# Performance work log

Hardware: AMD Instinct MI355X
Metric: run time of the kernel (lower is better)

The kernel has to match this reference:

```python
import jax, jax.numpy as jnp
import numpy as np

B, S, H, HF, V, L, NB, K = 8, 512, 1024, 512, 32000, 4, 8, 2
EPS = 1e-5


def _ln(x, g, b):
    m = jnp.mean(x, -1, keepdims=True)
    v = jnp.mean((x - m) ** 2, -1, keepdims=True)
    return (x - m) * jax.lax.rsqrt(v + EPS) * g + b


def setup_inputs() -> dict:
    key = jax.random.key(0)
    ks = jax.random.split(key, 12)
    n = lambda i, shape, s=0.02: jax.random.normal(ks[i], shape, jnp.float32) * s
    return {
        "input_ids": jax.random.randint(ks[0], (B, S), 0, V),
        "emb": n(1, (V, H)),
        "pos": n(2, (1, 512, H)),
        "torsion_field": jnp.zeros((1, H), jnp.float32),
        "lm_w": n(3, (H, V)),
        "lm_b": jnp.zeros((V,), jnp.float32),
        "sel_w": n(4, (L, H, NB)),
        "sel_b": jnp.zeros((L, NB), jnp.float32),
        "g1": jnp.ones((L, NB, H), jnp.float32),
        "b1": jnp.zeros((L, NB, H), jnp.float32),
        "attn_w": n(5, (L, NB, H, H)),
        "attn_b": jnp.zeros((L, NB, H), jnp.float32),
        "g2": jnp.ones((L, NB, H), jnp.float32),
        "b2": jnp.zeros((L, NB, H), jnp.float32),
        "ff1_w": n(6, (L, NB, H, HF)),
        "ff1_b": jnp.zeros((L, NB, HF), jnp.float32),
        "ff2_w": n(7, (L, NB, HF, H)),
        "ff2_b": jnp.zeros((L, NB, H), jnp.float32),
        "tg": n(8, (L, NB, H), 0.01),
    }


def _forward(input_ids, emb, pos, torsion_field, lm_w, lm_b, sel_w, sel_b,
             g1, b1, attn_w, attn_b, g2, b2, ff1_w, ff1_b, ff2_w, ff2_b, tg):
    # embedding + positional encoding
    h = emb[input_ids] + pos[:, :input_ids.shape[1], :]        # [B,S,H]
    tf = torsion_field[0]                                      # [H] (zeros buffer)
    PRIORITY = 0.5  # fresh block: success_rate*0.6 + excitement*0.4 = 0.5
    for l in range(L):
        # router: sigmoid(Linear(mean-pooled x)), mixed with block priority; topk on batch row 0
        scores = jax.nn.sigmoid(jnp.mean(h, 1) @ sel_w[l] + sel_b[l])   # [B,NB]
        adj0 = scores[0] * 0.7 + PRIORITY * 0.3                         # [NB]
        _, top_idx = jax.lax.top_k(adj0, K)                             # [K]
        params = jax.tree_util.tree_map(
            lambda p: p[l][top_idx],
            (g1, b1, attn_w, attn_b, g2, b2, ff1_w, ff1_b, ff2_w, ff2_b, tg))

        def blk(carry, p):
            pg1, pb1, pwa, pba, pg2, pb2, pw1, pbf1, pw2, pbf2, ptg = p
            x = carry
            ha = _ln(x, pg1, pb1) @ pwa + pba                           # [B,S,H]
            ha = ha * (1.0 + jax.nn.sigmoid(ptg) * tf)[None, None, :]
            hm = x + 0.5 * ha
            h2 = _ln(hm, pg2, pb2)
            h2 = jax.nn.gelu(h2 @ pw1 + pbf1, approximate=False) @ pw2 + pbf2
            return hm + 0.5 * h2, None

        h, _ = jax.lax.scan(blk, h, params)
        h = 1.5 * h  # h*0.5 + h after each layer
    return h @ lm_w + lm_b                                     # [B,S,V]


def reference(input_ids, emb, pos, torsion_field, lm_w, lm_b, sel_w, sel_b,
              g1, b1, attn_w, attn_b, g2, b2, ff1_w, ff1_b, ff2_w, ff2_b, tg):
    return _forward(input_ids, emb, pos, torsion_field, lm_w, lm_b, sel_w, sel_b,
                    g1, b1, attn_w, attn_b, g2, b2, ff1_w, ff1_b, ff2_w, ff2_b, tg)
```

## Files before the change

kernel.cpp:

```cpp
#include <hip/hip_runtime.h>


typedef unsigned short u16;
typedef short bf16x8 __attribute__((ext_vector_type(8)));
typedef float f32x4 __attribute__((ext_vector_type(4)));

struct __align__(8) u16x4_t { u16 x, y, z, w; };

#define MTOT 4096
#define HDIM 1024
#define HFF  512
#define VOC  32000
#define NLAYER 4
#define NBLK 8

#define VMW(n) asm volatile("s_waitcnt vmcnt(" #n ")" ::: "memory")
#define BARR() do { asm volatile("" ::: "memory"); __builtin_amdgcn_s_barrier(); asm volatile("" ::: "memory"); } while (0)

__device__ __forceinline__ u16 f2bf(float f) {
  unsigned u = __float_as_uint(f);
  unsigned r = u + 0x7FFFu + ((u >> 16) & 1u);
  return (u16)(r >> 16);
}

__device__ __forceinline__ float b2f(u16 v) {
  return __uint_as_float(((unsigned)v) << 16);
}

__device__ __forceinline__ float sigmoidf_(float z) {
  return 1.0f / (1.0f + expf(-z));
}

__device__ __forceinline__ void gload16(const void* g, void* l) {
  __builtin_amdgcn_global_load_lds(
      (const __attribute__((address_space(1))) void*)g,
      (__attribute__((address_space(3))) void*)l, 16, 0, 0);
}

__global__ void embed_lm_kernel(const int* __restrict__ ids,
                                const float* __restrict__ emb,
                                const float* __restrict__ pos,
                                u16* __restrict__ x,
                                const float* __restrict__ lm_w,
                                u16* __restrict__ lmT) {
  __shared__ float tile[32][33];
  int b = blockIdx.x, tid = threadIdx.x;
  if (b < MTOT) {
    int s = b & 511;
    int id = ids[b];
    float4 e = ((const float4*)(emb + (size_t)id * HDIM))[tid];
    float4 p = ((const float4*)(pos + (size_t)s * HDIM))[tid];
    u16x4_t r;
    r.x = f2bf(e.x + p.x); r.y = f2bf(e.y + p.y);
    r.z = f2bf(e.z + p.z); r.w = f2bf(e.w + p.w);
    ((u16x4_t*)(x + (size_t)b * HDIM))[tid] = r;
    return;
  }
  int c = b - MTOT;
  int n0 = (c % 1000) * 32, k0 = (c / 1000) * 32;
  int tx = tid & 31, ty = tid >> 5;
#pragma unroll
  for (int j = 0; j < 4; ++j) {
    int kr = k0 + ty + j * 8;
    tile[ty + j * 8][tx] = lm_w[(size_t)kr * VOC + n0 + tx];
  }
  __syncthreads();
#pragma unroll
  for (int j = 0; j < 4; ++j) {
    int nr = n0 + ty + j * 8;
    lmT[(size_t)nr * HDIM + k0 + tx] = f2bf(tile[tx][ty + j * 8]);
  }
}

__global__ void colsum_kernel(const u16* __restrict__ x, float* __restrict__ partial) {
  int j = blockIdx.x;
  int t = threadIdx.x;
  float4 s; s.x = 0.f; s.y = 0.f; s.z = 0.f; s.w = 0.f;
  for (int r = 0; r < 8; ++r) {
    u16x4_t a = ((const u16x4_t*)(x + (size_t)(j * 8 + r) * HDIM))[t];
    s.x += b2f(a.x); s.y += b2f(a.y); s.z += b2f(a.z); s.w += b2f(a.w);
  }
  ((float4*)(partial + (size_t)j * HDIM))[t] = s;
}

__global__ void router_finalize(const float* __restrict__ partial,
                                const float* __restrict__ selw,
                                const float* __restrict__ selb,
                                const float* __restrict__ tg_l,
                                const float* __restrict__ tf,
                                int* __restrict__ idx_out,
                                float* __restrict__ scale_out) {
  int t = threadIdx.x;
  float s = 0.f;
  for (int j = 0; j < 64; ++j) s += partial[(size_t)j * HDIM + t];
  float mean = s * (1.0f / 512.0f);
  __shared__ float sm[HDIM];
  __shared__ float sc[NBLK];
  __shared__ int sidx[2];
  sm[t] = mean;
  __syncthreads();
  int wave = t >> 6, lane = t & 63;
  if (wave < NBLK) {
    float p = 0.f;
    for (int h = lane; h < HDIM; h += 64) p += sm[h] * selw[h * NBLK + wave];
    for (int o = 32; o; o >>= 1) p += __shfl_down(p, o);
    if (lane == 0) sc[wave] = p;
  }
  __syncthreads();
  if (t == 0) {
    float adj[NBLK];
    for (int i = 0; i < NBLK; ++i) {
      float z = sc[i] + selb[i];
      adj[i] = sigmoidf_(z) * 0.7f + 0.15f;
    }
    int i0 = 0;
    for (int i = 1; i < NBLK; ++i) if (adj[i] > adj[i0]) i0 = i;
    int i1 = -1;
    for (int i = 0; i < NBLK; ++i) {
      if (i == i0) continue;
      if (i1 < 0 || adj[i] > adj[i1]) i1 = i;
    }
    idx_out[0] = i0; idx_out[1] = i1;
    sidx[0] = i0; sidx[1] = i1;
  }
  __syncthreads();
  for (int k = 0; k < 2; ++k) {
    int id = sidx[k];
    float z = tg_l[(size_t)id * HDIM + t];
    scale_out[k * HDIM + t] = 1.0f + sigmoidf_(z) * tf[t];
  }
}

__global__ void prep_kernel(const float* __restrict__ aw,
                            const float* __restrict__ f1w,
                            const float* __restrict__ f2w,
                            const int* __restrict__ idx, int slot,
                            u16* __restrict__ wA, u16* __restrict__ w1,
                            u16* __restrict__ w2,
                            const u16* __restrict__ x,
                            const float* __restrict__ g_base,
                            const float* __restrict__ b_base,
                            u16* __restrict__ abf) {
  __shared__ float sh[32 * 33];
  int b = blockIdx.x, tid = threadIdx.x;
  int id = idx[slot];
  if (b < 2048) {
    float (*tile)[33] = (float(*)[33])sh;
    const float* src; u16* dst; int K, N, n0, k0;
    if (b < 1024) {
      K = 1024; N = 1024; src = aw + (size_t)id * 1024 * 1024;
      n0 = (b & 31) * 32; k0 = (b >> 5) * 32; dst = wA;
    } else if (b < 1536) {
      int c = b - 1024; K = 1024; N = 512; src = f1w + (size_t)id * 1024 * 512;
      n0 = (c & 15) * 32; k0 = (c >> 4) * 32; dst = w1;
    } else {
      int c = b - 1536; K = 512; N = 1024; src = f2w + (size_t)id * 512 * 1024;
      n0 = (c & 31) * 32; k0 = (c >> 5) * 32; dst = w2;
    }
    int tx = tid & 31, ty = tid >> 5;
#pragma unroll
    for (int j = 0; j < 4; ++j) {
      int kr = k0 + ty + j * 8;
      tile[ty + j * 8][tx] = src[(size_t)kr * N + n0 + tx];
    }
    __syncthreads();
#pragma unroll
    for (int j = 0; j < 4; ++j) {
      int nr = n0 + ty + j * 8;
      dst[(size_t)nr * K + k0 + tx] = f2bf(tile[tx][ty + j * 8]);
    }
    return;
  }
  int row = b - 2048, t = tid;
  const float* g = g_base + (size_t)id * HDIM;
  const float* bb = b_base + (size_t)id * HDIM;
  u16x4_t xv = ((const u16x4_t*)(x + (size_t)row * HDIM))[t];
  float v0 = b2f(xv.x), v1 = b2f(xv.y), v2 = b2f(xv.z), v3 = b2f(xv.w);
  float s = v0 + v1 + v2 + v3;
  float q = v0 * v0 + v1 * v1 + v2 * v2 + v3 * v3;
  for (int o = 32; o; o >>= 1) { s += __shfl_down(s, o); q += __shfl_down(q, o); }
  float* ss = sh; float* sq = sh + 8;
  int wave = t >> 6, lane = t & 63;
  if (lane == 0) { ss[wave] = s; sq[wave] = q; }
  __syncthreads();
  if (t == 0) {
    float S = ss[0] + ss[1] + ss[2] + ss[3];
    float Q = sq[0] + sq[1] + sq[2] + sq[3];
    ss[0] = S * (1.0f / 1024.0f);
    sq[0] = Q * (1.0f / 1024.0f);
  }
  __syncthreads();
  float mean = ss[0];
  float var = sq[0] - mean * mean;
  float rs = rsqrtf(var + 1e-5f);
  float4 gv = ((const float4*)g)[t];
  float4 bv = ((const float4*)bb)[t];
  u16x4_t o4;
  o4.x = f2bf((v0 - mean) * rs * gv.x + bv.x);
  o4.y = f2bf((v1 - mean) * rs * gv.y + bv.y);
  o4.z = f2bf((v2 - mean) * rs * gv.z + bv.z);
  o4.w = f2bf((v3 - mean) * rs * gv.w + bv.w);
  ((u16x4_t*)(abf + (size_t)row * HDIM))[t] = o4;
}

__global__ void ln_kernel(const u16* __restrict__ x,
                          const float* __restrict__ g_base,
                          const float* __restrict__ b_base,
                          const int* __restrict__ idx_ptr, int slot,
                          u16* __restrict__ out) {
  int row = blockIdx.x, t = threadIdx.x;
  size_t off = (size_t)idx_ptr[slot] * HDIM;
  const float* g = g_base + off;
  const float* b = b_base + off;
  u16x4_t xv = ((const u16x4_t*)(x + (size_t)row * HDIM))[t];
  float v0 = b2f(xv.x), v1 = b2f(xv.y), v2 = b2f(xv.z), v3 = b2f(xv.w);
  float s = v0 + v1 + v2 + v3;
  float q = v0 * v0 + v1 * v1 + v2 * v2 + v3 * v3;
  for (int o = 32; o; o >>= 1) { s += __shfl_down(s, o); q += __shfl_down(q, o); }
  __shared__ float ss[4], sq[4];
  int wave = t >> 6, lane = t & 63;
  if (lane == 0) { ss[wave] = s; sq[wave] = q; }
  __syncthreads();
  if (t == 0) {
    float S = ss[0] + ss[1] + ss[2] + ss[3];
    float Q = sq[0] + sq[1] + sq[2] + sq[3];
    ss[0] = S * (1.0f / 1024.0f);
    sq[0] = Q * (1.0f / 1024.0f);
  }
  __syncthreads();
  float mean = ss[0];
  float var = sq[0] - mean * mean;
  float rs = rsqrtf(var + 1e-5f);
  float4 gv = ((const float4*)g)[t];
  float4 bv = ((const float4*)b)[t];
  u16x4_t o4;
  o4.x = f2bf((v0 - mean) * rs * gv.x + bv.x);
  o4.y = f2bf((v1 - mean) * rs * gv.y + bv.y);
  o4.z = f2bf((v2 - mean) * rs * gv.z + bv.z);
  o4.w = f2bf((v3 - mean) * rs * gv.w + bv.w);
  ((u16x4_t*)(out + (size_t)row * HDIM))[t] = o4;
}

template <int BM, int BN, int EPI>
__global__ __launch_bounds__(256) void gemm_layer(
    const u16* __restrict__ A, const u16* __restrict__ Bt, int N, int K,
    const float* __restrict__ bias_base, const int* __restrict__ idx_ptr,
    int slot, int bias_stride, const float* __restrict__ scale,
    u16* __restrict__ xres, u16* __restrict__ outb, float lscale) {
  constexpr int TM = BM / 2, TN = BN / 2;
  constexpr int FM = TM / 16, FN = TN / 16;
  constexpr int NLD = (BM + BN) / 16;
  __shared__ __align__(16) u16 lds[(BM + BN) * 128];

  const int tid = threadIdx.x, wave = tid >> 6, lane = tid & 63;
  const int m0 = blockIdx.y * BM, n0 = blockIdx.x * BN;
  const int wm = wave >> 1, wn = wave & 1;
  const int fr = lane & 15, g = lane >> 4;
  const float* bias =
      bias_base + (idx_ptr ? (size_t)idx_ptr[slot] * bias_stride : 0);

  const u16* gbase[NLD];
  unsigned ldsoff[NLD];
#pragma unroll
  for (int j = 0; j < NLD; ++j) {
    int lo = (tid + j * 256) * 16;
    int q = (lo >> 4) & 15;
    if (lo < BM * 256) {
      int row = lo >> 8;
      gbase[j] = A + (size_t)(m0 + row) * K + (q ^ (row & 7)) * 8;
    } else {
      int bo = lo - BM * 256;
      int row = bo >> 8;
      gbase[j] = Bt + (size_t)(n0 + row) * K + (q ^ (row & 7)) * 8;
    }
    ldsoff[j] = (unsigned)(lo >> 1);
  }

  unsigned offA[FM][4], offB[FN][4];
#pragma unroll
  for (int mi = 0; mi < FM; ++mi)
#pragma unroll
    for (int kk = 0; kk < 4; ++kk)
      offA[mi][kk] = (unsigned)((wm * TM + mi * 16 + fr) * 256 +
                                (((kk * 4 + g) ^ (fr & 7)) << 4));
#pragma unroll
  for (int ni = 0; ni < FN; ++ni)
#pragma unroll
    for (int kk = 0; kk < 4; ++kk)
      offB[ni][kk] = (unsigned)(BM * 256 + (wn * TN + ni * 16 + fr) * 256 +
                                (((kk * 4 + g) ^ (fr & 7)) << 4));

  f32x4 acc[FM][FN];
#pragma unroll
  for (int i = 0; i < FM; ++i)
#pragma unroll
    for (int j = 0; j < FN; ++j) acc[i][j] = (f32x4){0.f, 0.f, 0.f, 0.f};

  for (int kt = 0; kt < K; kt += 128) {
#pragma unroll
    for (int j = 0; j < NLD; ++j) gload16(gbase[j] + kt, lds + ldsoff[j]);
    __syncthreads();
#pragma unroll
    for (int kk = 0; kk < 4; ++kk) {
      bf16x8 af[FM], bf[FN];
#pragma unroll
      for (int mi = 0; mi < FM; ++mi)
        af[mi] = *(const bf16x8*)((const char*)lds + offA[mi][kk]);
#pragma unroll
      for (int ni = 0; ni < FN; ++ni)
        bf[ni] = *(const bf16x8*)((const char*)lds + offB[ni][kk]);
#pragma unroll
      for (int mi = 0; mi < FM; ++mi)
#pragma unroll
        for (int ni = 0; ni < FN; ++ni)
          acc[mi][ni] = __builtin_amdgcn_mfma_f32_16x16x32_bf16(
              af[mi], bf[ni], acc[mi][ni], 0, 0, 0);
    }
    __syncthreads();
  }

  const int rb = g * 4, cn = fr;
  float bvv[FN], svv[FN];
#pragma unroll
  for (int ni = 0; ni < FN; ++ni) {
    int n = n0 + wn * TN + ni * 16 + cn;
    bvv[ni] = bias[n];
    svv[ni] = (EPI == 0) ? scale[n] : 0.f;
  }
#pragma unroll
  for (int mi = 0; mi < FM; ++mi) {
#pragma unroll
    for (int r = 0; r < 4; ++r) {
      int m = m0 + wm * TM + mi * 16 + rb + r;
      size_t base = (size_t)m * N + n0 + wn * TN + cn;
#pragma unroll
      for (int ni = 0; ni < FN; ++ni) {
        float c = acc[mi][ni][r] + bvv[ni];
        size_t o = base + ni * 16;
        if (EPI == 0) {
          float xv = b2f(xres[o]);
          xres[o] = f2bf(xv + 0.5f * (c * svv[ni]));
        } else if (EPI == 1) {
          float ge = 0.5f * c * (1.0f + erff(c * 0.70710678118654752f));
          outb[o] = f2bf(ge);
        } else {
          float xv = b2f(xres[o]);
          xres[o] = f2bf((xv + 0.5f * c) * lscale);
        }
      }
    }
  }
}

__global__ __launch_bounds__(512, 2) void gemm_lm(
    const u16* __restrict__ A, const u16* __restrict__ Bt,
    const float* __restrict__ bias, float* __restrict__ out) {
  constexpr int K = HDIM;
  constexpr int N = VOC;
  constexpr int NT = K / 64;
  __shared__ __align__(16) u16 smbuf[2 * 32768];

  const int tid = threadIdx.x, wid = tid >> 6, lane = tid & 63;
  const int bid = blockIdx.x;
  const int vbid = (bid & 7) * 250 + (bid >> 3);
  const int n0 = (vbid >> 4) * 256;
  const int m0 = (vbid & 15) * 256;
  const int wm = wid >> 2, wn = wid & 3;
  const int fr = lane & 15, g = lane >> 4;

  const int r0 = tid >> 3, q = tid & 7;
  const int sg = (q ^ (r0 & 7)) * 8;
  const u16* usrc[4][2];
  unsigned uoff[4][2];
  usrc[0][0] = Bt + (size_t)(n0 + r0) * K + sg;        uoff[0][0] = 16384u + tid * 8;
  usrc[0][1] = Bt + (size_t)(n0 + 64 + r0) * K + sg;   uoff[0][1] = 20480u + tid * 8;
  usrc[1][0] = Bt + (size_t)(n0 + 128 + r0) * K + sg;  uoff[1][0] = 24576u + tid * 8;
  usrc[1][1] = Bt + (size_t)(n0 + 192 + r0) * K + sg;  uoff[1][1] = 28672u + tid * 8;
  usrc[2][0] = A + (size_t)(m0 + r0) * K + sg;         uoff[2][0] = 0u + tid * 8;
  usrc[2][1] = A + (size_t)(m0 + 128 + r0) * K + sg;   uoff[2][1] = 8192u + tid * 8;
  usrc[3][0] = A + (size_t)(m0 + 64 + r0) * K + sg;    uoff[3][0] = 4096u + tid * 8;
  usrc[3][1] = A + (size_t)(m0 + 192 + r0) * K + sg;   uoff[3][1] = 12288u + tid * 8;

  unsigned offA[8][2], offB[4][2];
#pragma unroll
  for (int mi = 0; mi < 8; ++mi)
#pragma unroll
    for (int kk = 0; kk < 2; ++kk)
      offA[mi][kk] = (unsigned)((wm * 128 + mi * 16 + fr) * 128 +
                                (((kk * 4 + g) ^ (fr & 7)) << 4));
#pragma unroll
  for (int ni = 0; ni < 4; ++ni)
#pragma unroll
    for (int kk = 0; kk < 2; ++kk)
      offB[ni][kk] = (unsigned)(32768 + (wn * 64 + ni * 16 + fr) * 128 +
                                (((kk * 4 + g) ^ (fr & 7)) << 4));

  f32x4 acc[8][4];
#pragma unroll
  for (int i = 0; i < 8; ++i)
#pragma unroll
    for (int j = 0; j < 4; ++j) acc[i][j] = (f32x4){0.f, 0.f, 0.f, 0.f};

#pragma unroll
  for (int u = 0; u < 4; ++u) {
    gload16(usrc[u][0], smbuf + uoff[u][0]);
    gload16(usrc[u][1], smbuf + uoff[u][1]);
  }

  for (int t = 0; t < NT; ++t) {
    const char* cb = (const char*)smbuf + (size_t)(t & 1) * 65536;
    u16* nb = smbuf + ((t + 1) & 1) * 32768;
    const int ko = (t + 1) * 64;
    const bool st = (t + 1 < NT);
    bf16x8 avl[4], avh[4], bv[4];
    VMW(2);
    BARR();
#pragma unroll
    for (int ni = 0; ni < 4; ++ni) bv[ni] = *(const bf16x8*)(cb + offB[ni][0]);
#pragma unroll
    for (int mi = 0; mi < 4; ++mi) avl[mi] = *(const bf16x8*)(cb + offA[mi][0]);
    if (st) {
      gload16(usrc[0][0] + ko, nb + uoff[0][0]);
      gload16(usrc[0][1] + ko, nb + uoff[0][1]);
    }
    __builtin_amdgcn_s_setprio(1);
#pragma unroll
    for (int mi = 0; mi < 4; ++mi)
#pragma unroll
      for (int ni = 0; ni < 4; ++ni)
        acc[mi][ni] = __builtin_amdgcn_mfma_f32_16x16x32_bf16(
            avl[mi], bv[ni], acc[mi][ni], 0, 0, 0);
    __builtin_amdgcn_s_setprio(0);
    if (t < NT - 1) { VMW(2); } else { VMW(0); }
    BARR();
#pragma unroll
    for (int mi = 0; mi < 4; ++mi)
      avh[mi] = *(const bf16x8*)(cb + offA[4 + mi][0]);
    if (st) {
      gload16(usrc[1][0] + ko, nb + uoff[1][0]);
      gload16(usrc[1][1] + ko, nb + uoff[1][1]);
    }
    __builtin_amdgcn_s_setprio(1);
#pragma unroll
    for (int mi = 0; mi < 4; ++mi)
#pragma unroll
      for (int ni = 0; ni < 4; ++ni)
        acc[4 + mi][ni] = __builtin_amdgcn_mfma_f32_16x16x32_bf16(
            avh[mi], bv[ni], acc[4 + mi][ni], 0, 0, 0);
    __builtin_amdgcn_s_setprio(0);
#pragma unroll
    for (int ni = 0; ni < 4; ++ni) bv[ni] = *(const bf16x8*)(cb + offB[ni][1]);
#pragma unroll
    for (int mi = 0; mi < 4; ++mi) avl[mi] = *(const bf16x8*)(cb + offA[mi][1]);
    if (st) {
      gload16(usrc[2][0] + ko, nb + uoff[2][0]);
      gload16(usrc[2][1] + ko, nb + uoff[2][1]);
    }
    __builtin_amdgcn_s_setprio(1);
#pragma unroll
    for (int mi = 0; mi < 4; ++mi)
#pragma unroll
      for (int ni = 0; ni < 4; ++ni)
        acc[mi][ni] = __builtin_amdgcn_mfma_f32_16x16x32_bf16(
            avl[mi], bv[ni], acc[mi][ni], 0, 0, 0);
    __builtin_amdgcn_s_setprio(0);
#pragma unroll
    for (int mi = 0; mi < 4; ++mi)
      avh[mi] = *(const bf16x8*)(cb + offA[4 + mi][1]);
    if (st) {
      gload16(usrc[3][0] + ko, nb + uoff[3][0]);
      gload16(usrc[3][1] + ko, nb + uoff[3][1]);
    }
    __builtin_amdgcn_s_setprio(1);
#pragma unroll
    for (int mi = 0; mi < 4; ++mi)
#pragma unroll
      for (int ni = 0; ni < 4; ++ni)
        acc[4 + mi][ni] = __builtin_amdgcn_mfma_f32_16x16x32_bf16(
            avh[mi], bv[ni], acc[4 + mi][ni], 0, 0, 0);
    __builtin_amdgcn_s_setprio(0);
  }

  const int rb = g * 4, cn = fr;
  float bvv[4];
#pragma unroll
  for (int ni = 0; ni < 4; ++ni) bvv[ni] = bias[n0 + wn * 64 + ni * 16 + cn];
#pragma unroll
  for (int mi = 0; mi < 8; ++mi) {
#pragma unroll
    for (int r = 0; r < 4; ++r) {
      int m = m0 + wm * 128 + mi * 16 + rb + r;
      float* orow = out + (size_t)m * N + n0 + wn * 64 + cn;
#pragma unroll
      for (int ni = 0; ni < 4; ++ni)
        __builtin_nontemporal_store(acc[mi][ni][r] + bvv[ni], orow + ni * 16);
    }
  }
}

extern "C" void kernel_launch(void* const* d_in, const int* in_sizes, int n_in,
                              void* d_out, int out_size, void* d_ws,
                              size_t ws_size, hipStream_t stream) {
  (void)in_sizes; (void)n_in; (void)out_size; (void)ws_size;
  const int*   ids    = (const int*)d_in[0];
  const float* emb    = (const float*)d_in[1];
  const float* pos    = (const float*)d_in[2];
  const float* tf     = (const float*)d_in[3];
  const float* lm_w   = (const float*)d_in[4];
  const float* lm_b   = (const float*)d_in[5];
  const float* sel_w  = (const float*)d_in[6];
  const float* sel_b  = (const float*)d_in[7];
  const float* g1     = (const float*)d_in[8];
  const float* b1     = (const float*)d_in[9];
  const float* attn_w = (const float*)d_in[10];
  const float* attn_b = (const float*)d_in[11];
  const float* g2     = (const float*)d_in[12];
  const float* b2     = (const float*)d_in[13];
  const float* ff1_w  = (const float*)d_in[14];
  const float* ff1_b  = (const float*)d_in[15];
  const float* ff2_w  = (const float*)d_in[16];
  const float* ff2_b  = (const float*)d_in[17];
  const float* tg     = (const float*)d_in[18];
  float* out = (float*)d_out;

  char* ws = (char*)d_ws;
  u16*   x       = (u16*)(ws + 0);
  u16*   abf     = (u16*)(ws + 16777216);
  u16*   tbuf    = (u16*)(ws + 25165824);
  u16*   wA      = (u16*)(ws + 29360128);
  u16*   w1      = (u16*)(ws + 31457280);
  u16*   w2      = (u16*)(ws + 32505856);
  u16*   lmT     = (u16*)(ws + 33554432);
  float* partial = (float*)(ws + 99090432);
  float* scalev  = (float*)(ws + 99352576);
  int*   idx     = (int*)(ws + 99360768);

  embed_lm_kernel<<<MTOT + VOC, 256, 0, stream>>>(ids, emb, pos, x, lm_w, lmT);

  for (int l = 0; l < NLAYER; ++l) {
    colsum_kernel<<<64, 256, 0, stream>>>(x, partial);
    router_finalize<<<1, 1024, 0, stream>>>(
        partial, sel_w + (size_t)l * HDIM * NBLK, sel_b + l * NBLK,
        tg + (size_t)l * NBLK * HDIM, tf, idx, scalev);
    const float* aw_l  = attn_w + (size_t)l * NBLK * HDIM * HDIM;
    const float* f1w_l = ff1_w + (size_t)l * NBLK * HDIM * HFF;
    const float* f2w_l = ff2_w + (size_t)l * NBLK * HFF * HDIM;
    for (int k = 0; k < 2; ++k) {
      prep_kernel<<<2048 + MTOT, 256, 0, stream>>>(
          aw_l, f1w_l, f2w_l, idx, k, wA, w1, w2, x,
          g1 + (size_t)l * NBLK * HDIM, b1 + (size_t)l * NBLK * HDIM, abf);
      gemm_layer<128, 64, 0><<<dim3(16, 32), 256, 0, stream>>>(
          abf, wA, HDIM, HDIM, attn_b + (size_t)l * NBLK * HDIM, idx, k, HDIM,
          scalev + k * HDIM, x, nullptr, 1.0f);
      ln_kernel<<<MTOT, 256, 0, stream>>>(x, g2 + (size_t)l * NBLK * HDIM,
                                          b2 + (size_t)l * NBLK * HDIM, idx, k,
                                          abf);
      gemm_layer<64, 64, 1><<<dim3(8, 64), 256, 0, stream>>>(
          abf, w1, HFF, HDIM, ff1_b + (size_t)l * NBLK * HFF, idx, k, HFF,
          nullptr, nullptr, tbuf, 1.0f);
      float lsc = (k == 1) ? 1.5f : 1.0f;
      gemm_layer<128, 64, 2><<<dim3(16, 32), 256, 0, stream>>>(
          tbuf, w2, HDIM, HFF, ff2_b + (size_t)l * NBLK * HDIM, idx, k, HDIM,
          nullptr, x, nullptr, lsc);
    }
  }

  gemm_lm<<<2000, 512, 0, stream>>>(x, lmT, lm_b, out);
}
```

Measured before the change: 931.7 us.

## Shrink LM-head GEMM tile to 128x128 with simpler double-buffered pipeline

```diff
diff --git a/kernel.cpp b/kernel.cpp
--- a/kernel.cpp
+++ b/kernel.cpp
@@ -352,133 +352,109 @@
   }
 }
 
-__global__ __launch_bounds__(512, 2) void gemm_lm(
+__global__ __launch_bounds__(256, 2) void gemm_lm(
     const u16* __restrict__ A, const u16* __restrict__ Bt,
     const float* __restrict__ bias, float* __restrict__ out) {
   constexpr int K = HDIM;
   constexpr int N = VOC;
   constexpr int NT = K / 64;
-  __shared__ __align__(16) u16 smbuf[2 * 32768];
-
-  const int tid = threadIdx.x, wid = tid >> 6, lane = tid & 63;
+  __shared__ __align__(16) u16 smbuf[2 * 16384];
+
+  const int tid = threadIdx.x, wave = tid >> 6, lane = tid & 63;
   const int bid = blockIdx.x;
-  const int vbid = (bid & 7) * 250 + (bid >> 3);
-  const int n0 = (vbid >> 4) * 256;
-  const int m0 = (vbid & 15) * 256;
-  const int wm = wid >> 2, wn = wid & 3;
+  const int vbid = (bid & 7) * 1000 + (bid >> 3);
+  const int n0 = (vbid >> 5) * 128;
+  const int m0 = (vbid & 31) * 128;
+  const int wm = wave >> 1, wn = wave & 1;
   const int fr = lane & 15, g = lane >> 4;
 
-  const int r0 = tid >> 3, q = tid & 7;
-  const int sg = (q ^ (r0 & 7)) * 8;
-  const u16* usrc[4][2];
-  unsigned uoff[4][2];
-  usrc[0][0] = Bt + (size_t)(n0 + r0) * K + sg;        uoff[0][0] = 16384u + tid * 8;
-  usrc[0][1] = Bt + (size_t)(n0 + 64 + r0) * K + sg;   uoff[0][1] = 20480u + tid * 8;
-  usrc[1][0] = Bt + (size_t)(n0 + 128 + r0) * K + sg;  uoff[1][0] = 24576u + tid * 8;
-  usrc[1][1] = Bt + (size_t)(n0 + 192 + r0) * K + sg;  uoff[1][1] = 28672u + tid * 8;
-  usrc[2][0] = A + (size_t)(m0 + r0) * K + sg;         uoff[2][0] = 0u + tid * 8;
-  usrc[2][1] = A + (size_t)(m0 + 128 + r0) * K + sg;   uoff[2][1] = 8192u + tid * 8;
-  usrc[3][0] = A + (size_t)(m0 + 64 + r0) * K + sg;    uoff[3][0] = 4096u + tid * 8;
-  usrc[3][1] = A + (size_t)(m0 + 192 + r0) * K + sg;   uoff[3][1] = 12288u + tid * 8;
-
-  unsigned offA[8][2], offB[4][2];
-#pragma unroll
-  for (int mi = 0; mi < 8; ++mi)
+  const u16* gb[8];
+  unsigned lso[8];
+#pragma unroll
+  for (int j = 0; j < 8; ++j) {
+    int lo = (tid + j * 256) * 16;
+    int q = (lo >> 4) & 7;
+    if (lo < 16384) {
+      int row = lo >> 7;
+      gb[j] = A + (size_t)(m0 + row) * K + (q ^ (row & 7)) * 8;
+    } else {
+      int bo = lo - 16384;
+      int row = bo >> 7;
+      gb[j] = Bt + (size_t)(n0 + row) * K + (q ^ (row & 7)) * 8;
+    }
+    lso[j] = (unsigned)(lo >> 1);
+  }
+
+  unsigned offA[4][2], offB[4][2];
+#pragma unroll
+  for (int mi = 0; mi < 4; ++mi)
 #pragma unroll
     for (int kk = 0; kk < 2; ++kk)
-      offA[mi][kk] = (unsigned)((wm * 128 + mi * 16 + fr) * 128 +
+      offA[mi][kk] = (unsigned)((wm * 64 + mi * 16 + fr) * 128 +
                                 (((kk * 4 + g) ^ (fr & 7)) << 4));
 #pragma unroll
   for (int ni = 0; ni < 4; ++ni)
 #pragma unroll
     for (int kk = 0; kk < 2; ++kk)
-      offB[ni][kk] = (unsigned)(32768 + (wn * 64 + ni * 16 + fr) * 128 +
+      offB[ni][kk] = (unsigned)(16384 + (wn * 64 + ni * 16 + fr) * 128 +
                                 (((kk * 4 + g) ^ (fr & 7)) << 4));
 
-  f32x4 acc[8][4];
-#pragma unroll
-  for (int i = 0; i < 8; ++i)
+  f32x4 acc[4][4];
+#pragma unroll
+  for (int i = 0; i < 4; ++i)
 #pragma unroll
     for (int j = 0; j < 4; ++j) acc[i][j] = (f32x4){0.f, 0.f, 0.f, 0.f};
 
 #pragma unroll
-  for (int u = 0; u < 4; ++u) {
-    gload16(usrc[u][0], smbuf + uoff[u][0]);
-    gload16(usrc[u][1], smbuf + uoff[u][1]);
-  }
+  for (int j = 0; j < 8; ++j) gload16(gb[j], smbuf + lso[j]);
 
   for (int t = 0; t < NT; ++t) {
-    const char* cb = (const char*)smbuf + (size_t)(t & 1) * 65536;
-    u16* nb = smbuf + ((t + 1) & 1) * 32768;
+    const char* cb = (const char*)smbuf + (size_t)(t & 1) * 32768;
+    u16* nb = smbuf + ((t + 1) & 1) * 16384;
     const int ko = (t + 1) * 64;
-    const bool st = (t + 1 < NT);
-    bf16x8 avl[4], avh[4], bv[4];
-    VMW(2);
     BARR();
-#pragma unroll
-    for (int ni = 0; ni < 4; ++ni) bv[ni] = *(const bf16x8*)(cb + offB[ni][0]);
-#pragma unroll
-    for (int mi = 0; mi < 4; ++mi) avl[mi] = *(const bf16x8*)(cb + offA[mi][0]);
-    if (st) {
-      gload16(usrc[0][0] + ko, nb + uoff[0][0]);
-      gload16(usrc[0][1] + ko, nb + uoff[0][1]);
-    }
-    __builtin_amdgcn_s_setprio(1);
-#pragma unroll
-    for (int mi = 0; mi < 4; ++mi)
+    if (t + 1 < NT) {
+#pragma unroll
+      for (int j = 0; j < 8; ++j) gload16(gb[j] + ko, nb + lso[j]);
+      VMW(8);
+    } else {
+      VMW(0);
+    }
+    BARR();
+    {
+      bf16x8 af[4], bf[4];
+#pragma unroll
+      for (int mi = 0; mi < 4; ++mi)
+        af[mi] = *(const bf16x8*)(cb + offA[mi][0]);
 #pragma unroll
       for (int ni = 0; ni < 4; ++ni)
-        acc[mi][ni] = __builtin_amdgcn_mfma_f32_16x16x32_bf16(
-            avl[mi], bv[ni], acc[mi][ni], 0, 0, 0);
-    __builtin_amdgcn_s_setprio(0);
-    if (t < NT - 1) { VMW(2); } else { VMW(0); }
-    BARR();
-#pragma unroll
-    for (int mi = 0; mi < 4; ++mi)
-      avh[mi] = *(const bf16x8*)(cb + offA[4 + mi][0]);
-    if (st) {
-      gload16(usrc[1][0] + ko, nb + uoff[1][0]);
-      gload16(usrc[1][1] + ko, nb + uoff[1][1]);
-    }
-    __builtin_amdgcn_s_setprio(1);
-#pragma unroll
-    for (int mi = 0; mi < 4; ++mi)
+        bf[ni] = *(const bf16x8*)(cb + offB[ni][0]);
+      __builtin_amdgcn_s_setprio(1);
+#pragma unroll
+      for (int mi = 0; mi < 4; ++mi)
+#pragma unroll
+        for (int ni = 0; ni < 4; ++ni)
+          acc[mi][ni] = __builtin_amdgcn_mfma_f32_16x16x32_bf16(
+              af[mi], bf[ni], acc[mi][ni], 0, 0, 0);
+      __builtin_amdgcn_s_setprio(0);
+    }
+    {
+      bf16x8 af[4], bf[4];
+#pragma unroll
+      for (int mi = 0; mi < 4; ++mi)
+        af[mi] = *(const bf16x8*)(cb + offA[mi][1]);
 #pragma unroll
       for (int ni = 0; ni < 4; ++ni)
-        acc[4 + mi][ni] = __builtin_amdgcn_mfma_f32_16x16x32_bf16(
-            avh[mi], bv[ni], acc[4 + mi][ni], 0, 0, 0);
-    __builtin_amdgcn_s_setprio(0);
-#pragma unroll
-    for (int ni = 0; ni < 4; ++ni) bv[ni] = *(const bf16x8*)(cb + offB[ni][1]);
-#pragma unroll
-    for (int mi = 0; mi < 4; ++mi) avl[mi] = *(const bf16x8*)(cb + offA[mi][1]);
-    if (st) {
-      gload16(usrc[2][0] + ko, nb + uoff[2][0]);
-      gload16(usrc[2][1] + ko, nb + uoff[2][1]);
-    }
-    __builtin_amdgcn_s_setprio(1);
-#pragma unroll
-    for (int mi = 0; mi < 4; ++mi)
-#pragma unroll
-      for (int ni = 0; ni < 4; ++ni)
-        acc[mi][ni] = __builtin_amdgcn_mfma_f32_16x16x32_bf16(
-            avl[mi], bv[ni], acc[mi][ni], 0, 0, 0);
-    __builtin_amdgcn_s_setprio(0);
-#pragma unroll
-    for (int mi = 0; mi < 4; ++mi)
-      avh[mi] = *(const bf16x8*)(cb + offA[4 + mi][1]);
-    if (st) {
-      gload16(usrc[3][0] + ko, nb + uoff[3][0]);
-      gload16(usrc[3][1] + ko, nb + uoff[3][1]);
-    }
-    __builtin_amdgcn_s_setprio(1);
-#pragma unroll
-    for (int mi = 0; mi < 4; ++mi)
-#pragma unroll
-      for (int ni = 0; ni < 4; ++ni)
-        acc[4 + mi][ni] = __builtin_amdgcn_mfma_f32_16x16x32_bf16(
-            avh[mi], bv[ni], acc[4 + mi][ni], 0, 0, 0);
-    __builtin_amdgcn_s_setprio(0);
+        bf[ni] = *(const bf16x8*)(cb + offB[ni][1]);
+      __builtin_amdgcn_s_setprio(1);
+#pragma unroll
+      for (int mi = 0; mi < 4; ++mi)
+#pragma unroll
+        for (int ni = 0; ni < 4; ++ni)
+          acc[mi][ni] = __builtin_amdgcn_mfma_f32_16x16x32_bf16(
+              af[mi], bf[ni], acc[mi][ni], 0, 0, 0);
+      __builtin_amdgcn_s_setprio(0);
+    }
   }
 
   const int rb = g * 4, cn = fr;
@@ -486,10 +462,10 @@
 #pragma unroll
   for (int ni = 0; ni < 4; ++ni) bvv[ni] = bias[n0 + wn * 64 + ni * 16 + cn];
 #pragma unroll
-  for (int mi = 0; mi < 8; ++mi) {
+  for (int mi = 0; mi < 4; ++mi) {
 #pragma unroll
     for (int r = 0; r < 4; ++r) {
-      int m = m0 + wm * 128 + mi * 16 + rb + r;
+      int m = m0 + wm * 64 + mi * 16 + rb + r;
       float* orow = out + (size_t)m * N + n0 + wn * 64 + cn;
 #pragma unroll
       for (int ni = 0; ni < 4; ++ni)
@@ -565,5 +541,5 @@
     }
   }
 
-  gemm_lm<<<2000, 512, 0, stream>>>(x, lmT, lm_b, out);
-}
+  gemm_lm<<<8000, 256, 0, stream>>>(x, lmT, lm_b, out);
+}
```

Result: slower. 1.051 ms (+12.8%).
